# Kernel tuning notes

Measured on AMD Instinct MI355X. Metric: run time of the kernel, lower is better.

## Reference

```python
import jax, jax.numpy as jnp
import numpy as np

EMBED_DIM = 768
NUM_HEADS = 12
HEAD_DIM = EMBED_DIM // NUM_HEADS
SCALE = HEAD_DIM ** -0.5


def setup_inputs() -> dict:
    key = jax.random.key(0)
    k1, k2, k3, k4, k5 = jax.random.split(key, 5)
    B, T = 8, 1024
    init = 0.02
    return {
        "hidden_states": jax.random.normal(k1, (B, T, EMBED_DIM), dtype=jnp.float32),
        "qkv_w": jax.random.normal(k2, (EMBED_DIM, 3 * EMBED_DIM), dtype=jnp.float32) * init,
        "qkv_b": jnp.zeros((3 * EMBED_DIM,), dtype=jnp.float32),
        "proj_w": jax.random.normal(k3, (EMBED_DIM, EMBED_DIM), dtype=jnp.float32) * init,
        "proj_b": jnp.zeros((EMBED_DIM,), dtype=jnp.float32),
    }


def reference(hidden_states, qkv_w, qkv_b, proj_w, proj_b):
    B, T, E = hidden_states.shape
    # fused QKV projection: [B, T, 3E] -> [3, B, H, T, Dh]
    mixed = hidden_states @ qkv_w + qkv_b
    mixed = mixed.reshape(B, T, 3, NUM_HEADS, HEAD_DIM).transpose(2, 0, 3, 1, 4)
    q, k, v = mixed[0], mixed[1], mixed[2]
    # scores: [B, H, T, T]
    scores = jnp.einsum("bhqd,bhkd->bhqk", q, k) * SCALE
    probs = jax.nn.softmax(scores, axis=-1)
    # context: [B, T, H, Dh] -> [B, T, E]
    ctx = jnp.einsum("bhqk,bhkd->bqhd", probs, v).reshape(B, T, E)
    return ctx @ proj_w + proj_b
```

## Files before the change

kernel.cpp:

```cpp
#include <hip/hip_runtime.h>
#include <hip/hip_bf16.h>

#define B_ 8
#define T_ 1024
#define E_ 768
#define H_ 12
#define DH_ 64
#define E3_ 2304
#define M_ (B_ * T_)
#define SCALE_LOG2E 0.18033688011112042f

typedef __attribute__((ext_vector_type(8))) short short8;
typedef __attribute__((ext_vector_type(4))) float float4_;
typedef __attribute__((ext_vector_type(4))) unsigned short ushort4_;

__device__ __forceinline__ unsigned short f2bf(float f) {
    union { float f; unsigned int u; } v; v.f = f;
    unsigned int r = v.u + 0x7fffu + ((v.u >> 16) & 1u);
    return (unsigned short)(r >> 16);
}

__device__ __forceinline__ unsigned int pk_bf16(float a, float b) {
    float2 t; t.x = a; t.y = b;
    union { __hip_bfloat162 h; unsigned int u; } cv;
    cv.h = __float22bfloat162_rn(t);
    return cv.u;
}

__device__ __forceinline__ void gld_lds16(const unsigned short* g, unsigned short* l) {
    __builtin_amdgcn_global_load_lds(
        (const __attribute__((address_space(1))) void*)g,
        (__attribute__((address_space(3))) void*)l,
        16, 0, 0);
}

__global__ __launch_bounds__(256) void prep(const float* __restrict__ hs,
                                            const float* __restrict__ qkv_w,
                                            const float* __restrict__ proj_w,
                                            unsigned short* __restrict__ hs_bf,
                                            unsigned short* __restrict__ qkvwT,
                                            unsigned short* __restrict__ projwT) {
    __shared__ float tile[32][33];
    const int id = blockIdx.x;
    const int tid = threadIdx.x;
    if (id < 6144) {
        const int i = (id * 256 + tid) * 4;
        float4_ v = *(const float4_*)(hs + i);
        ushort4_ o;
        o.x = f2bf(v.x); o.y = f2bf(v.y); o.z = f2bf(v.z); o.w = f2bf(v.w);
        *(ushort4_*)(hs_bf + i) = o;
        return;
    }
    const float* W; unsigned short* Wt; int N, bx, by;
    if (id < 6144 + 1728) {
        const int t = id - 6144; W = qkv_w; Wt = qkvwT; N = E3_;
        bx = t % 72; by = t / 72;
    } else {
        const int t = id - 7872; W = proj_w; Wt = projwT; N = E_;
        bx = t % 24; by = t / 24;
    }
    const int k0 = by * 32, n0 = bx * 32;
    const int tx = tid & 31, ty = tid >> 5;
    for (int i = ty; i < 32; i += 8)
        tile[i][tx] = W[(size_t)(k0 + i) * N + n0 + tx];
    __syncthreads();
    for (int i = ty; i < 32; i += 8)
        Wt[(size_t)(n0 + i) * E_ + k0 + tx] = f2bf(tile[tx][i]);
}

template <int STORE_MODE>
__global__ __launch_bounds__(256) void gemm_mfma(const unsigned short* __restrict__ A,
                                                 const unsigned short* __restrict__ Wt,
                                                 const float* __restrict__ bias,
                                                 void* __restrict__ Cout,
                                                 unsigned short* __restrict__ Vt,
                                                 int M, int N, int K) {
    __shared__ __align__(16) unsigned short Al[2][128 * 32];
    __shared__ __align__(16) unsigned short Wl[2][128 * 32];

    const int tid = threadIdx.x;
    const int lane = tid & 63;
    const int w = tid >> 6;

    const int id = blockIdx.x;
    const int xcd = id & 7;
    const int slot = id >> 3;
    const int bx = slot >> 3;
    const int by = xcd * 8 + (slot & 7);
    const int bm = by * 128;
    const int bn = bx * 128;

    const int wm = (w >> 1) * 64;
    const int wn = (w & 1) * 64;
    const int quad = lane >> 4;
    const int l16 = lane & 15;

    const int srow = w * 32 + (lane >> 2);
    const int schunk = (lane & 3) * 8;
    const int sbase = w * 32 * 32 + lane * 8;

    const unsigned short* ga = A + (size_t)(bm + srow) * K + schunk;
    const unsigned short* gw = Wt + (size_t)(bn + srow) * K + schunk;

    float4_ acc[4][4] = {};

    gld_lds16(ga, &Al[0][sbase]);
    gld_lds16(ga + (size_t)16 * K, &Al[0][sbase + 512]);
    gld_lds16(gw, &Wl[0][sbase]);
    gld_lds16(gw + (size_t)16 * K, &Wl[0][sbase + 512]);

    const int NI = K >> 5;
    for (int i = 0; i < NI; ++i) {
        const int cur = i & 1;
        __syncthreads();
        if (i + 1 < NI) {
            const unsigned short* ga2 = ga + (size_t)(i + 1) * 32;
            const unsigned short* gw2 = gw + (size_t)(i + 1) * 32;
            const int nxt = cur ^ 1;
            gld_lds16(ga2, &Al[nxt][sbase]);
            gld_lds16(ga2 + (size_t)16 * K, &Al[nxt][sbase + 512]);
            gld_lds16(gw2, &Wl[nxt][sbase]);
            gld_lds16(gw2 + (size_t)16 * K, &Wl[nxt][sbase + 512]);
        }
        short8 af[4], bf[4];
#pragma unroll
        for (int mt = 0; mt < 4; ++mt)
            af[mt] = *(const short8*)(&Al[cur][(wm + mt * 16 + l16) * 32 + quad * 8]);
#pragma unroll
        for (int nt = 0; nt < 4; ++nt)
            bf[nt] = *(const short8*)(&Wl[cur][(wn + nt * 16 + l16) * 32 + quad * 8]);
#pragma unroll
        for (int mt = 0; mt < 4; ++mt)
#pragma unroll
            for (int nt = 0; nt < 4; ++nt)
                acc[mt][nt] = __builtin_amdgcn_mfma_f32_16x16x32_bf16(af[mt], bf[nt],
                                                                      acc[mt][nt], 0, 0, 0);
    }

    {
#pragma unroll
        for (int nt = 0; nt < 4; ++nt) {
            const int col = bn + wn + nt * 16 + l16;
            const float bv = bias[col];
#pragma unroll
            for (int mt = 0; mt < 4; ++mt) {
#pragma unroll
                for (int i = 0; i < 4; ++i) {
                    const int row = bm + wm + mt * 16 + quad * 4 + i;
                    const float v = acc[mt][nt][i] + bv;
                    if (STORE_MODE >= 1)
                        ((unsigned short*)Cout)[(size_t)row * N + col] = f2bf(v);
                    else
                        ((float*)Cout)[(size_t)row * N + col] = v;
                }
            }
        }
    }
    (void)Vt;
}

__global__ __launch_bounds__(512, 2) void gemm288(const unsigned short* __restrict__ A,
                                                  const unsigned short* __restrict__ Wt,
                                                  const float* __restrict__ bias,
                                                  unsigned short* __restrict__ mixedOut,
                                                  unsigned short* __restrict__ Vt) {
    const int K = 768;
    const int NT = 12;
    __shared__ __align__(16) unsigned short lds[70144];

    const int tid = threadIdx.x;
    const int lane = tid & 63;
    const int w = tid >> 6;
    const int quad = lane >> 4;
    const int l16 = lane & 15;
    const int wM = w >> 1;
    const int wN = w & 1;

    const int id = blockIdx.x;
    const int xcd = id & 7;
    const int slot = id >> 3;
    const int bx = slot >> 2;
    const int byl = slot & 3;
    const int bm = (xcd * 4 + byl) * 256;
    const int bn = bx * 288;

    const int j4 = (w < 4) ? (w + 32) : 36;
    int kk0 = ((w % 18) / 6) * 64 + w;
    int kk1 = (((w + 8) % 18) / 6) * 64 + (w + 8);
    int kk2 = (((w + 16) % 18) / 6) * 64 + (w + 16);
    int kk3 = (((w + 24) % 18) / 6) * 64 + (w + 24);
    int kk4 = (j4 >= 36) ? (3 * 64 + 36) : (((j4 % 18) / 6) * 64 + j4);
#define CS_(a, b) { int _lo = min(a, b), _hi = max(a, b); a = _lo; b = _hi; }
    CS_(kk0, kk1) CS_(kk3, kk4) CS_(kk2, kk4) CS_(kk2, kk3) CS_(kk1, kk4)
    CS_(kk0, kk3) CS_(kk0, kk2) CS_(kk1, kk3) CS_(kk1, kk2)
#undef CS_
    const int b0 = kk0 & 63, b1 = kk1 & 63, b2 = kk2 & 63, b3 = kk3 & 63, b4 = kk4 & 63;

    const int srcrow = lane >> 3;
    const int ssw = ((lane & 7) ^ (srcrow & 7)) << 3;
    const unsigned short* gaL = A + (size_t)(bm + srcrow) * K + ssw;
    const unsigned short* gbL = Wt + (size_t)(bn + srcrow) * K + ssw;
    unsigned short* ldsl = lds + lane * 8;

    const int rsw0 = ((quad) ^ (l16 & 7)) << 3;
    const int rsw1 = ((quad + 4) ^ (l16 & 7)) << 3;
    const unsigned short* rdA = lds + (wM * 64 + l16) * 64;
    const unsigned short* rdB = lds + 32768 + (wN * 144 + l16) * 64;

    short8 aF[4][2], bF[3][2];
    float4_ acc[4][9] = {};

#define STA_(aj, toff, bufA) gld_lds16(gaL + (size_t)(aj) * 6144 + (toff), (bufA) + (aj) * 512)
#define STB_(j, toff, bufB) { \
    const int _j = (j); \
    const unsigned short* _s = gbL + (size_t)(_j >= 36 ? 0 : _j) * 6144 + (toff); \
    unsigned short* _d = (_j >= 36) ? (ldsl + 69632) : ((bufB) + _j * 512); \
    gld_lds16(_s, _d); }

#define LDA_(buf) { \
    const unsigned short* _a = rdA + (buf) * 16384; \
    aF[0][0] = *(const short8*)(_a + rsw0);        aF[0][1] = *(const short8*)(_a + rsw1); \
    aF[1][0] = *(const short8*)(_a + 1024 + rsw0); aF[1][1] = *(const short8*)(_a + 1024 + rsw1); \
    aF[2][0] = *(const short8*)(_a + 2048 + rsw0); aF[2][1] = *(const short8*)(_a + 2048 + rsw1); \
    aF[3][0] = *(const short8*)(_a + 3072 + rsw0); aF[3][1] = *(const short8*)(_a + 3072 + rsw1); }

#define LDB_(buf, nh) { \
    const unsigned short* _b = rdB + (buf) * 18432 + (nh) * 3072; \
    bF[0][0] = *(const short8*)(_b + rsw0);        bF[0][1] = *(const short8*)(_b + rsw1); \
    bF[1][0] = *(const short8*)(_b + 1024 + rsw0); bF[1][1] = *(const short8*)(_b + 1024 + rsw1); \
    bF[2][0] = *(const short8*)(_b + 2048 + rsw0); bF[2][1] = *(const short8*)(_b + 2048 + rsw1); }

#define MMA_(nh) \
    __builtin_amdgcn_s_setprio(1); \
    _Pragma("unroll") for (int mt = 0; mt < 4; ++mt) \
    _Pragma("unroll") for (int nt = 0; nt < 3; ++nt) { \
        acc[mt][(nh) * 3 + nt] = __builtin_amdgcn_mfma_f32_16x16x32_bf16( \
            aF[mt][0], bF[nt][0], acc[mt][(nh) * 3 + nt], 0, 0, 0); \
        acc[mt][(nh) * 3 + nt] = __builtin_amdgcn_mfma_f32_16x16x32_bf16( \
            aF[mt][1], bF[nt][1], acc[mt][(nh) * 3 + nt], 0, 0, 0); } \
    __builtin_amdgcn_s_setprio(0);

#define BARRIER_ __builtin_amdgcn_s_barrier()
#define WLGKM0_ { asm volatile("s_waitcnt lgkmcnt(0)" ::: "memory"); __builtin_amdgcn_sched_barrier(0); }
#define WVM3_ asm volatile("s_waitcnt vmcnt(3)" ::: "memory")
#define WVM0_ asm volatile("s_waitcnt vmcnt(0)" ::: "memory")

    {
        unsigned short* bufA = ldsl;
        unsigned short* bufB = ldsl + 32768;
        STA_(w, 0, bufA); STA_(w + 8, 0, bufA); STA_(w + 16, 0, bufA); STA_(w + 24, 0, bufA);
        STB_(b0, 0, bufB); STB_(b1, 0, bufB); STB_(b2, 0, bufB); STB_(b3, 0, bufB); STB_(b4, 0, bufB);
    }
    WVM3_; BARRIER_;

#pragma unroll 1
    for (int t = 0; t < NT - 1; ++t) {
        const int buf = t & 1;
        const int toff = (t + 1) * 64;
        unsigned short* bufA = ldsl + (buf ^ 1) * 16384;
        unsigned short* bufB = ldsl + 32768 + (buf ^ 1) * 18432;

        LDA_(buf); LDB_(buf, 0);
        STA_(w, toff, bufA); STA_(w + 8, toff, bufA); STA_(w + 16, toff, bufA);
        BARRIER_; WLGKM0_; MMA_(0);
        WVM3_; BARRIER_;
        LDB_(buf, 1);
        STA_(w + 24, toff, bufA); STB_(b0, toff, bufB); STB_(b1, toff, bufB);
        BARRIER_; WLGKM0_; MMA_(1);
        WVM3_; BARRIER_;
        LDB_(buf, 2);
        STB_(b2, toff, bufB); STB_(b3, toff, bufB); STB_(b4, toff, bufB);
        BARRIER_; WLGKM0_; MMA_(2);
        WVM3_; BARRIER_;
    }
    {
        LDA_(1); LDB_(1, 0);
        BARRIER_; WLGKM0_; MMA_(0);
        WVM0_; BARRIER_;
        LDB_(1, 1);
        BARRIER_; WLGKM0_; MMA_(1);
        BARRIER_;
        LDB_(1, 2);
        BARRIER_; WLGKM0_; MMA_(2);
    }
#undef STA_
#undef STB_
#undef LDA_
#undef LDB_
#undef MMA_

    const int bb = bm >> 10;
    const int tloc = (bm & 1023) + wM * 64;
#pragma unroll
    for (int ntg = 0; ntg < 9; ++ntg) {
        const int col = bn + wN * 144 + ntg * 16 + l16;
        const float bv = bias[col];
        if (col >= 1536) {
            const int n = col - 1536;
            const int h = n >> 6, d = n & 63;
            const size_t vrow = (size_t)((bb * H_ + h) * 64 + d) * T_;
#pragma unroll
            for (int mt = 0; mt < 4; ++mt) {
                uint2 pk;
                pk.x = pk_bf16(acc[mt][ntg][0] + bv, acc[mt][ntg][1] + bv);
                pk.y = pk_bf16(acc[mt][ntg][2] + bv, acc[mt][ntg][3] + bv);
                *(uint2*)(Vt + vrow + tloc + mt * 16 + quad * 4) = pk;
            }
        } else {
            const float qs = (col < 768) ? SCALE_LOG2E : 1.0f;
#pragma unroll
            for (int mt = 0; mt < 4; ++mt) {
#pragma unroll
                for (int i = 0; i < 4; ++i) {
                    const int row = bm + wM * 64 + mt * 16 + quad * 4 + i;
                    mixedOut[(size_t)row * E3_ + col] = f2bf((acc[mt][ntg][i] + bv) * qs);
                }
            }
        }
    }
}

__global__ __launch_bounds__(256) void attn_mfma(const unsigned short* __restrict__ mixed,
                                                 const unsigned short* __restrict__ Vt,
                                                 unsigned short* __restrict__ ctx) {
    const int bh = blockIdx.x;
    const int b = bh / H_;
    const int h = bh % H_;
    const int q0 = blockIdx.y * 128;
    const int tid = threadIdx.x;
    const int lane = tid & 63;
    const int w = tid >> 6;
    const int quad = lane >> 4;
    const int l16 = lane & 15;

    __shared__ __align__(16) unsigned short Kl[8 * 520];
    __shared__ __align__(16) unsigned short Vl[8 * 520];
    __shared__ __align__(16) unsigned short Pl[4][32 * 72];
    unsigned short* pw = &Pl[w][0];

    short8 qf[2][2];
#pragma unroll
    for (int hh = 0; hh < 2; ++hh) {
        const size_t qrow = (size_t)(b * T_ + q0 + w * 32 + hh * 16 + l16) * E3_ + h * 64;
        qf[hh][0] = *(const short8*)(mixed + qrow + quad * 8);
        qf[hh][1] = *(const short8*)(mixed + qrow + 32 + quad * 8);
    }

    float4_ o[2][4] = {};
    float lps[2] = {0.0f, 0.0f};

    const size_t kbase = (size_t)(b * T_) * E3_ + E_ + h * 64;
    const size_t vtb = (size_t)bh * 64 * T_;

    const int srow = tid >> 3;
    const int sc = tid & 7;

    for (int kv0 = 0; kv0 < T_; kv0 += 64) {
        short8 k1 = *(const short8*)(mixed + kbase + (size_t)(kv0 + srow) * E3_ + sc * 8);
        short8 k2 = *(const short8*)(mixed + kbase + (size_t)(kv0 + srow + 32) * E3_ + sc * 8);
        short8 v1 = *(const short8*)(Vt + vtb + (size_t)srow * T_ + kv0 + sc * 8);
        short8 v2 = *(const short8*)(Vt + vtb + (size_t)(srow + 32) * T_ + kv0 + sc * 8);
        __syncthreads();
        *(short8*)(&Kl[sc * 520 + srow * 8]) = k1;
        *(short8*)(&Kl[sc * 520 + (srow + 32) * 8]) = k2;
        *(short8*)(&Vl[sc * 520 + srow * 8]) = v1;
        *(short8*)(&Vl[sc * 520 + (srow + 32) * 8]) = v2;
        __syncthreads();

        float4_ st[2][4];
#pragma unroll
        for (int nt = 0; nt < 4; ++nt) {
            const int key = nt * 16 + l16;
            short8 kf0 = *(const short8*)(&Kl[quad * 520 + key * 8]);
            short8 kf1 = *(const short8*)(&Kl[(4 + quad) * 520 + key * 8]);
#pragma unroll
            for (int hh = 0; hh < 2; ++hh) {
                float4_ z = {};
                z = __builtin_amdgcn_mfma_f32_16x16x32_bf16(kf0, qf[hh][0], z, 0, 0, 0);
                st[hh][nt] = __builtin_amdgcn_mfma_f32_16x16x32_bf16(kf1, qf[hh][1], z, 0, 0, 0);
            }
        }

#pragma unroll
        for (int hh = 0; hh < 2; ++hh) {
#pragma unroll
            for (int nt = 0; nt < 4; ++nt) {
                const float p0 = __builtin_amdgcn_exp2f(st[hh][nt][0]);
                const float p1 = __builtin_amdgcn_exp2f(st[hh][nt][1]);
                const float p2 = __builtin_amdgcn_exp2f(st[hh][nt][2]);
                const float p3 = __builtin_amdgcn_exp2f(st[hh][nt][3]);
                uint2 pk;
                pk.x = pk_bf16(p0, p1);
                pk.y = pk_bf16(p2, p3);
                lps[hh] += (p0 + p1) + (p2 + p3);
                *(uint2*)(&pw[(hh * 16 + l16) * 72 + nt * 16 + quad * 4]) = pk;
            }
        }

        short8 pf[2][2];
#pragma unroll
        for (int hh = 0; hh < 2; ++hh) {
            pf[hh][0] = *(const short8*)(&pw[(hh * 16 + l16) * 72 + quad * 8]);
            pf[hh][1] = *(const short8*)(&pw[(hh * 16 + l16) * 72 + 32 + quad * 8]);
        }

#pragma unroll
        for (int dt = 0; dt < 4; ++dt) {
            const int d = dt * 16 + l16;
            short8 vf0 = *(const short8*)(&Vl[quad * 520 + d * 8]);
            short8 vf1 = *(const short8*)(&Vl[(4 + quad) * 520 + d * 8]);
#pragma unroll
            for (int hh = 0; hh < 2; ++hh) {
                o[hh][dt] = __builtin_amdgcn_mfma_f32_16x16x32_bf16(pf[hh][0], vf0, o[hh][dt], 0, 0, 0);
                o[hh][dt] = __builtin_amdgcn_mfma_f32_16x16x32_bf16(pf[hh][1], vf1, o[hh][dt], 0, 0, 0);
            }
        }
    }

#pragma unroll
    for (int hh = 0; hh < 2; ++hh) {
        float l = lps[hh];
        l += __shfl_xor(l, 16, 64);
        l += __shfl_xor(l, 32, 64);
        float4_ inv;
#pragma unroll
        for (int i = 0; i < 4; ++i)
            inv[i] = 1.0f / __shfl(l, quad * 4 + i, 16);
#pragma unroll
        for (int dt = 0; dt < 4; ++dt) {
#pragma unroll
            for (int i = 0; i < 4; ++i) {
                const float v = o[hh][dt][i] * inv[i];
                const size_t row = (size_t)(b * T_ + q0 + w * 32 + hh * 16 + quad * 4 + i);
                ctx[row * E_ + h * 64 + dt * 16 + l16] = f2bf(v);
            }
        }
    }
}

extern "C" void kernel_launch(void* const* d_in, const int* in_sizes, int n_in,
                              void* d_out, int out_size, void* d_ws, size_t ws_size,
                              hipStream_t stream) {
    const float* hs     = (const float*)d_in[0];
    const float* qkv_w  = (const float*)d_in[1];
    const float* qkv_b  = (const float*)d_in[2];
    const float* proj_w = (const float*)d_in[3];
    const float* proj_b = (const float*)d_in[4];
    float* out = (float*)d_out;

    unsigned short* hs_bf  = (unsigned short*)d_ws;
    unsigned short* qkvwT  = hs_bf + (size_t)M_ * E_;
    unsigned short* projwT = qkvwT + (size_t)E3_ * E_;
    unsigned short* mixed  = projwT + (size_t)E_ * E_;
    unsigned short* Vt     = mixed + (size_t)M_ * E3_;
    unsigned short* ctx    = hs_bf;

    prep<<<8448, 256, 0, stream>>>(hs, qkv_w, proj_w, hs_bf, qkvwT, projwT);

    gemm288<<<256, 512, 0, stream>>>(hs_bf, qkvwT, qkv_b, mixed, Vt);
    attn_mfma<<<dim3(B_ * H_, T_ / 128), 256, 0, stream>>>(mixed, Vt, ctx);
    gemm_mfma<0><<<(E_ / 128) * (M_ / 128), 256, 0, stream>>>(ctx, projwT, proj_b,
                                                              (void*)out, nullptr, M_, E_, E_);
}
```

Baseline: 177.9 us.

## Load K/V MFMA fragments directly from global memory, dropping LDS staging

Each wave now loads its K and V MFMA operand fragments straight from global memory into registers, removing the shared-memory K/V tiles and both block-wide barriers per KV step. It also raises wave priority around the MFMA blocks with s_setprio. In exchange, every one of the four waves in a block fetches the same K/V data separately, so it relies on cache hits. The global loads are also less coalesced (16-byte pieces from strided rows), and there is no explicit prefetch to hide latency.

```diff
diff --git a/kernel.cpp b/kernel.cpp
--- a/kernel.cpp
+++ b/kernel.cpp
@@ -333,8 +333,6 @@
     const int quad = lane >> 4;
     const int l16 = lane & 15;
 
-    __shared__ __align__(16) unsigned short Kl[8 * 520];
-    __shared__ __align__(16) unsigned short Vl[8 * 520];
     __shared__ __align__(16) unsigned short Pl[4][32 * 72];
     unsigned short* pw = &Pl[w][0];
 
@@ -351,35 +349,40 @@
 
     const size_t kbase = (size_t)(b * T_) * E3_ + E_ + h * 64;
     const size_t vtb = (size_t)bh * 64 * T_;
-
-    const int srow = tid >> 3;
-    const int sc = tid & 7;
+    const unsigned short* kb[4];
+    const unsigned short* vb[4];
+#pragma unroll
+    for (int nt = 0; nt < 4; ++nt)
+        kb[nt] = mixed + kbase + (size_t)(nt * 16 + l16) * E3_ + quad * 8;
+#pragma unroll
+    for (int dt = 0; dt < 4; ++dt)
+        vb[dt] = Vt + vtb + (size_t)(dt * 16 + l16) * T_ + quad * 8;
 
     for (int kv0 = 0; kv0 < T_; kv0 += 64) {
-        short8 k1 = *(const short8*)(mixed + kbase + (size_t)(kv0 + srow) * E3_ + sc * 8);
-        short8 k2 = *(const short8*)(mixed + kbase + (size_t)(kv0 + srow + 32) * E3_ + sc * 8);
-        short8 v1 = *(const short8*)(Vt + vtb + (size_t)srow * T_ + kv0 + sc * 8);
-        short8 v2 = *(const short8*)(Vt + vtb + (size_t)(srow + 32) * T_ + kv0 + sc * 8);
-        __syncthreads();
-        *(short8*)(&Kl[sc * 520 + srow * 8]) = k1;
-        *(short8*)(&Kl[sc * 520 + (srow + 32) * 8]) = k2;
-        *(short8*)(&Vl[sc * 520 + srow * 8]) = v1;
-        *(short8*)(&Vl[sc * 520 + (srow + 32) * 8]) = v2;
-        __syncthreads();
+        short8 kf[4][2], vf[4][2];
+#pragma unroll
+        for (int nt = 0; nt < 4; ++nt) {
+            kf[nt][0] = *(const short8*)(kb[nt]);
+            kf[nt][1] = *(const short8*)(kb[nt] + 32);
+        }
+#pragma unroll
+        for (int dt = 0; dt < 4; ++dt) {
+            vf[dt][0] = *(const short8*)(vb[dt]);
+            vf[dt][1] = *(const short8*)(vb[dt] + 32);
+        }
 
         float4_ st[2][4];
+        __builtin_amdgcn_s_setprio(1);
 #pragma unroll
         for (int nt = 0; nt < 4; ++nt) {
-            const int key = nt * 16 + l16;
-            short8 kf0 = *(const short8*)(&Kl[quad * 520 + key * 8]);
-            short8 kf1 = *(const short8*)(&Kl[(4 + quad) * 520 + key * 8]);
 #pragma unroll
             for (int hh = 0; hh < 2; ++hh) {
                 float4_ z = {};
-                z = __builtin_amdgcn_mfma_f32_16x16x32_bf16(kf0, qf[hh][0], z, 0, 0, 0);
-                st[hh][nt] = __builtin_amdgcn_mfma_f32_16x16x32_bf16(kf1, qf[hh][1], z, 0, 0, 0);
-            }
-        }
+                z = __builtin_amdgcn_mfma_f32_16x16x32_bf16(kf[nt][0], qf[hh][0], z, 0, 0, 0);
+                st[hh][nt] = __builtin_amdgcn_mfma_f32_16x16x32_bf16(kf[nt][1], qf[hh][1], z, 0, 0, 0);
+            }
+        }
+        __builtin_amdgcn_s_setprio(0);
 
 #pragma unroll
         for (int hh = 0; hh < 2; ++hh) {
@@ -404,17 +407,21 @@
             pf[hh][1] = *(const short8*)(&pw[(hh * 16 + l16) * 72 + 32 + quad * 8]);
         }
 
+        __builtin_amdgcn_s_setprio(1);
 #pragma unroll
         for (int dt = 0; dt < 4; ++dt) {
-            const int d = dt * 16 + l16;
-            short8 vf0 = *(const short8*)(&Vl[quad * 520 + d * 8]);
-            short8 vf1 = *(const short8*)(&Vl[(4 + quad) * 520 + d * 8]);
 #pragma unroll
             for (int hh = 0; hh < 2; ++hh) {
-                o[hh][dt] = __builtin_amdgcn_mfma_f32_16x16x32_bf16(pf[hh][0], vf0, o[hh][dt], 0, 0, 0);
-                o[hh][dt] = __builtin_amdgcn_mfma_f32_16x16x32_bf16(pf[hh][1], vf1, o[hh][dt], 0, 0, 0);
-            }
-        }
+                o[hh][dt] = __builtin_amdgcn_mfma_f32_16x16x32_bf16(pf[hh][0], vf[dt][0], o[hh][dt], 0, 0, 0);
+                o[hh][dt] = __builtin_amdgcn_mfma_f32_16x16x32_bf16(pf[hh][1], vf[dt][1], o[hh][dt], 0, 0, 0);
+            }
+        }
+        __builtin_amdgcn_s_setprio(0);
+
+#pragma unroll
+        for (int nt = 0; nt < 4; ++nt) kb[nt] += (size_t)64 * E3_;
+#pragma unroll
+        for (int dt = 0; dt < 4; ++dt) vb[dt] += 64;
     }
 
 #pragma unroll
```

Result: slower. 231.8 us (+30.3%).
